# Kernel tuning notes

Hardware: AMD Instinct MI355X
Metric: run time of the kernel (lower is better)

Reference implementation:

```python
import jax, jax.numpy as jnp
import numpy as np

N = 50000
E = 600000
D_IN, D_HID, D_OUT = 128, 128, 64


def gcn_conv(x, edge_index, W, b):
    """PyG GCNConv: add self-loops, symmetric deg^{-1/2} normalization,
    linear transform, scatter-add aggregation, bias."""
    n = x.shape[0]
    loop = jnp.arange(n, dtype=edge_index.dtype)
    src = jnp.concatenate([edge_index[0], loop])
    dst = jnp.concatenate([edge_index[1], loop])
    h = x @ W  # [N, out]
    deg = jax.ops.segment_sum(jnp.ones_like(dst, dtype=h.dtype), dst, num_segments=n)
    dinv = jnp.where(deg > 0, jax.lax.rsqrt(jnp.maximum(deg, 1e-12)), 0.0)
    norm = dinv[src] * dinv[dst]  # [E+N]
    msg = h[src] * norm[:, None]  # gather + scale
    out = jax.ops.segment_sum(msg, dst, num_segments=n)  # scatter-add
    return out + b


def setup_inputs() -> dict:
    key = jax.random.key(0)
    k1, k2, k3, k4 = jax.random.split(key, 4)
    x = jax.random.normal(k1, (N, D_IN), dtype=jnp.float32)
    edge_index = jax.random.randint(k2, (2, E), 0, N, dtype=jnp.int64)
    s1 = (1.0 / np.sqrt(D_IN)).astype(np.float32) if False else np.float32(1.0 / np.sqrt(D_IN))
    s2 = np.float32(1.0 / np.sqrt(D_HID))
    W1 = jax.random.normal(k3, (D_IN, D_HID), dtype=jnp.float32) * s1
    b1 = jnp.zeros((D_HID,), dtype=jnp.float32)
    W2 = jax.random.normal(k4, (D_HID, D_OUT), dtype=jnp.float32) * s2
    b2 = jnp.zeros((D_OUT,), dtype=jnp.float32)
    return {"x": x, "edge_index": edge_index, "W1": W1, "b1": b1, "W2": W2, "b2": b2}


def reference(x, edge_index, W1, b1, W2, b2):
    # eval mode: dropout p = 0
    h = jax.nn.relu(gcn_conv(x, edge_index, W1, b1))
    return gcn_conv(h, edge_index, W2, b2)
```

## Files before the change

kernel.cpp:

```cpp
#include <hip/hip_runtime.h>
#include <hip/hip_fp16.h>
#include <stdint.h>

#define DIN 128
#define DHID 128
#define DOUT2 64

typedef __attribute__((ext_vector_type(8))) short short8v;
typedef __attribute__((ext_vector_type(4))) float f32x4;

__device__ __forceinline__ unsigned short f2bf(float f) {
    unsigned u = __float_as_uint(f);
    u += 0x7fffu + ((u >> 16) & 1u);
    return (unsigned short)(u >> 16);
}
__device__ __forceinline__ float bf2f(unsigned short b) {
    return __uint_as_float(((unsigned)b) << 16);
}
__device__ __forceinline__ float bflo(unsigned v) { return __uint_as_float(v << 16); }
__device__ __forceinline__ float bfhi(unsigned v) { return __uint_as_float(v & 0xffff0000u); }
__device__ __forceinline__ unsigned short f2h(float f) {
    return __half_as_ushort(__float2half_rn(f));
}
__device__ __forceinline__ float h2f(unsigned bits) {
    return __half2float(__ushort_as_half((unsigned short)bits));
}

__device__ __forceinline__ int detect_mode(const unsigned* ei) {
    int lane = threadIdx.x & 63;
    unsigned hi = ei[2 * lane + 1];
    return (__ballot(hi == 0u) == ~0ull) ? 1 : 0;
}

__global__ void prep_kernel(const float* __restrict__ W1, const float* __restrict__ W2,
                            unsigned short* __restrict__ wt1, unsigned short* __restrict__ wt2,
                            const int* ei32, const long long* ei64, unsigned* deg, int E) {
    if (blockIdx.x == 0) {
        for (int idx = threadIdx.x; idx < 128 * 128; idx += 256) {
            int n = idx & 127, k = idx >> 7;
            wt1[n * 128 + k] = f2bf(W1[idx]);
        }
    } else if (blockIdx.x == 1) {
        for (int idx = threadIdx.x; idx < 128 * 64; idx += 256) {
            int n = idx & 63, k = idx >> 6;
            wt2[n * 128 + k] = f2bf(W2[idx]);
        }
    } else {
        int mode = detect_mode((const unsigned*)ei32);
        int e = (blockIdx.x - 2) * 256 + threadIdx.x;
        if (e < E) {
            int d = mode ? (int)ei64[(size_t)E + e] : ei32[(size_t)E + e];
            atomicAdd(&deg[d], 1u);
        }
    }
}

template <int DO, typename AT>
__global__ __launch_bounds__(256) void gemm_mfma_kernel(const AT* __restrict__ A,
                                                        const unsigned short* __restrict__ Wt,
                                                        unsigned short* __restrict__ out,
                                                        int M) {
    constexpr int NT = DO / 16;
    __shared__ unsigned short As[64 * 136];
    const int tid = threadIdx.x;
    const int row0 = blockIdx.x * 64;

    if constexpr (sizeof(AT) == 4) {
        for (int idx = tid; idx < 64 * 32; idx += 256) {
            int r = idx >> 5, c4 = idx & 31;
            int row = row0 + r;
            ushort4 o = {0, 0, 0, 0};
            if (row < M) {
                float4 v = ((const float4*)A)[(size_t)row * 32 + c4];
                o.x = f2bf(v.x);
                o.y = f2bf(v.y);
                o.z = f2bf(v.z);
                o.w = f2bf(v.w);
            }
            *(ushort4*)&As[r * 136 + c4 * 4] = o;
        }
    } else {
        for (int idx = tid; idx < 64 * 16; idx += 256) {
            int r = idx >> 4, c8 = idx & 15;
            int row = row0 + r;
            uint4 v = {0u, 0u, 0u, 0u};
            if (row < M) v = ((const uint4*)A)[(size_t)row * 16 + c8];
            *(uint4*)&As[r * 136 + c8 * 8] = v;
        }
    }
    __syncthreads();

    const int wid = tid >> 6, lane = tid & 63;
    const int r16 = lane & 15, g = lane >> 4;
    f32x4 acc[NT];
#pragma unroll
    for (int n = 0; n < NT; n++) acc[n] = (f32x4){0.f, 0.f, 0.f, 0.f};

    const unsigned short* a_base = &As[(wid * 16 + r16) * 136 + g * 8];
    const unsigned short* b_base = Wt + r16 * 128 + g * 8;
#pragma unroll
    for (int kk = 0; kk < 4; kk++) {
        short8v a = *(const short8v*)(a_base + kk * 32);
#pragma unroll
        for (int n = 0; n < NT; n++) {
            short8v b = *(const short8v*)(b_base + n * 16 * 128 + kk * 32);
            acc[n] = __builtin_amdgcn_mfma_f32_16x16x32_bf16(a, b, acc[n], 0, 0, 0);
        }
    }

    const int rbase = row0 + wid * 16 + g * 4;
#pragma unroll
    for (int n = 0; n < NT; n++) {
#pragma unroll
        for (int q = 0; q < 4; q++) {
            int row = rbase + q;
            if (row < M) out[(size_t)row * DO + n * 16 + r16] = f2bf(acc[n][q]);
        }
    }
}

__global__ __launch_bounds__(256) void scan_blocksum_kernel(const unsigned* deg, int* bsum,
                                                            float* dinv, int N) {
    __shared__ int s[256];
    int t = threadIdx.x;
    int base = blockIdx.x * 1024 + t * 4;
    int sum = 0;
    if (base + 3 < N) {
        int4 v = *(const int4*)((const int*)deg + base);
        sum = v.x + v.y + v.z + v.w;
        float4 dv;
        dv.x = rsqrtf((float)(v.x + 1));
        dv.y = rsqrtf((float)(v.y + 1));
        dv.z = rsqrtf((float)(v.z + 1));
        dv.w = rsqrtf((float)(v.w + 1));
        *(float4*)(dinv + base) = dv;
    } else {
        for (int j = 0; j < 4; j++)
            if (base + j < N) {
                int d = (int)deg[base + j];
                sum += d;
                dinv[base + j] = rsqrtf((float)(d + 1));
            }
    }
    s[t] = sum;
    __syncthreads();
    for (int off = 128; off > 0; off >>= 1) {
        if (t < off) s[t] += s[t + off];
        __syncthreads();
    }
    if (t == 0) bsum[blockIdx.x] = s[0];
}

__global__ __launch_bounds__(256) void scan_bsum_kernel(int* bsum, int* row_ptr, int nb, int N) {
    __shared__ int s[256];
    int t = threadIdx.x;
    int v = (t < nb) ? bsum[t] : 0;
    s[t] = v;
    __syncthreads();
    for (int off = 1; off < 256; off <<= 1) {
        int u = (t >= off) ? s[t - off] : 0;
        __syncthreads();
        s[t] += u;
        __syncthreads();
    }
    if (t < nb) bsum[t] = s[t] - v;
    if (t == 255) row_ptr[N] = s[255];
}

__global__ __launch_bounds__(256) void scan_write_kernel(const unsigned* deg, const int* bsum,
                                                         int* row_ptr, int* cursor, int N) {
    __shared__ int s[256];
    int t = threadIdx.x;
    int base = blockIdx.x * 1024 + t * 4;
    int d[4];
    int sum = 0;
#pragma unroll
    for (int j = 0; j < 4; j++) {
        int idx = base + j;
        d[j] = (idx < N) ? (int)deg[idx] : 0;
        sum += d[j];
    }
    s[t] = sum;
    __syncthreads();
    for (int off = 1; off < 256; off <<= 1) {
        int u = (t >= off) ? s[t - off] : 0;
        __syncthreads();
        s[t] += u;
        __syncthreads();
    }
    int run = bsum[blockIdx.x] + s[t] - sum;
#pragma unroll
    for (int j = 0; j < 4; j++) {
        int idx = base + j;
        if (idx < N) {
            row_ptr[idx] = run;
            cursor[idx] = run;
            run += d[j];
        }
    }
}

__global__ void scatter_pack32_kernel(const int* ei32, const long long* ei64, const float* dinv,
                                      int* cursor, unsigned* csr, int E) {
    int mode = detect_mode((const unsigned*)ei32);
    int e = blockIdx.x * blockDim.x + threadIdx.x;
    if (e >= E) return;
    int s, d;
    if (mode) {
        s = (int)ei64[e];
        d = (int)ei64[(size_t)E + e];
    } else {
        s = ei32[e];
        d = ei32[(size_t)E + e];
    }
    int pos = atomicAdd(&cursor[d], 1);
    csr[pos] = (unsigned)s | ((unsigned)f2h(dinv[s]) << 16);
}

__global__ void scatter_pack64_kernel(const int* ei32, const long long* ei64, const float* dinv,
                                      int* cursor, unsigned long long* csr, int E) {
    int mode = detect_mode((const unsigned*)ei32);
    int e = blockIdx.x * blockDim.x + threadIdx.x;
    if (e >= E) return;
    int s, d;
    if (mode) {
        s = (int)ei64[e];
        d = (int)ei64[(size_t)E + e];
    } else {
        s = ei32[e];
        d = ei32[(size_t)E + e];
    }
    int pos = atomicAdd(&cursor[d], 1);
    csr[pos] = (unsigned long long)(unsigned)s |
               ((unsigned long long)__float_as_uint(dinv[s]) << 32);
}

__device__ __forceinline__ void unpack(unsigned p, int& s, float& w) {
    s = (int)(p & 0xffffu);
    w = h2f(p >> 16);
}
__device__ __forceinline__ void unpack(unsigned long long p, int& s, float& w) {
    s = (int)(unsigned)(p & 0xffffffffu);
    w = __uint_as_float((unsigned)(p >> 32));
}

template <int D, bool RELU, typename OT, typename CT>
__global__ __launch_bounds__(256) void agg_kernel(const unsigned short* __restrict__ h,
                                                  const CT* __restrict__ csr,
                                                  const int* __restrict__ row_ptr,
                                                  const float* __restrict__ dinv,
                                                  const float* __restrict__ bias,
                                                  OT* __restrict__ out, int N) {
    const int wid = threadIdx.x >> 6;
    const int lane = threadIdx.x & 63;
    const int i = blockIdx.x * 4 + wid;
    if (i >= N) return;
    const float di = dinv[i];
    const int start = row_ptr[i], end = row_ptr[i + 1];

    if constexpr (D == 128) {
        const unsigned* hu = (const unsigned*)h;
        unsigned sv = hu[(size_t)i * 64 + lane];
        float a0 = di * bflo(sv), b0 = di * bfhi(sv);
        float a1 = 0.f, b1 = 0.f, a2 = 0.f, b2 = 0.f, a3 = 0.f, b3 = 0.f;
        int j = start;
        for (; j + 8 <= end; j += 8) {
            int s[8];
            float w[8];
            unsigned v[8];
#pragma unroll
            for (int u = 0; u < 8; u++) unpack(csr[j + u], s[u], w[u]);
#pragma unroll
            for (int u = 0; u < 8; u++) v[u] = hu[(size_t)s[u] * 64 + lane];
            a0 = fmaf(w[0], bflo(v[0]), a0);
            b0 = fmaf(w[0], bfhi(v[0]), b0);
            a1 = fmaf(w[1], bflo(v[1]), a1);
            b1 = fmaf(w[1], bfhi(v[1]), b1);
            a2 = fmaf(w[2], bflo(v[2]), a2);
            b2 = fmaf(w[2], bfhi(v[2]), b2);
            a3 = fmaf(w[3], bflo(v[3]), a3);
            b3 = fmaf(w[3], bfhi(v[3]), b3);
            a0 = fmaf(w[4], bflo(v[4]), a0);
            b0 = fmaf(w[4], bfhi(v[4]), b0);
            a1 = fmaf(w[5], bflo(v[5]), a1);
            b1 = fmaf(w[5], bfhi(v[5]), b1);
            a2 = fmaf(w[6], bflo(v[6]), a2);
            b2 = fmaf(w[6], bfhi(v[6]), b2);
            a3 = fmaf(w[7], bflo(v[7]), a3);
            b3 = fmaf(w[7], bfhi(v[7]), b3);
        }
        for (; j < end; ++j) {
            int s0;
            float w0;
            unpack(csr[j], s0, w0);
            unsigned v0 = hu[(size_t)s0 * 64 + lane];
            a0 = fmaf(w0, bflo(v0), a0);
            b0 = fmaf(w0, bfhi(v0), b0);
        }
        float2 bv = ((const float2*)bias)[lane];
        float rx = di * ((a0 + a1) + (a2 + a3)) + bv.x;
        float ry = di * ((b0 + b1) + (b2 + b3)) + bv.y;
        if (RELU) {
            rx = fmaxf(rx, 0.f);
            ry = fmaxf(ry, 0.f);
        }
        if constexpr (sizeof(OT) == 2) {
            unsigned pv = (unsigned)f2bf(rx) | ((unsigned)f2bf(ry) << 16);
            ((unsigned*)out)[(size_t)i * 64 + lane] = pv;
        } else {
            ((float2*)out)[(size_t)i * 64 + lane] = make_float2(rx, ry);
        }
    } else {
        float a0 = di * bf2f(h[(size_t)i * 64 + lane]);
        float a1 = 0.f, a2 = 0.f, a3 = 0.f;
        int j = start;
        for (; j + 8 <= end; j += 8) {
            int s[8];
            float w[8];
            float v[8];
#pragma unroll
            for (int u = 0; u < 8; u++) unpack(csr[j + u], s[u], w[u]);
#pragma unroll
            for (int u = 0; u < 8; u++) v[u] = bf2f(h[(size_t)s[u] * 64 + lane]);
            a0 = fmaf(w[0], v[0], a0);
            a1 = fmaf(w[1], v[1], a1);
            a2 = fmaf(w[2], v[2], a2);
            a3 = fmaf(w[3], v[3], a3);
            a0 = fmaf(w[4], v[4], a0);
            a1 = fmaf(w[5], v[5], a1);
            a2 = fmaf(w[6], v[6], a2);
            a3 = fmaf(w[7], v[7], a3);
        }
        for (; j < end; ++j) {
            int s0;
            float w0;
            unpack(csr[j], s0, w0);
            a0 = fmaf(w0, bf2f(h[(size_t)s0 * 64 + lane]), a0);
        }
        float r = di * ((a0 + a1) + (a2 + a3)) + bias[lane];
        if (RELU) r = fmaxf(r, 0.f);
        if constexpr (sizeof(OT) == 2) {
            out[(size_t)i * 64 + lane] = (OT)f2bf(r);
        } else {
            out[(size_t)i * 64 + lane] = r;
        }
    }
}

extern "C" void kernel_launch(void* const* d_in, const int* in_sizes, int n_in,
                              void* d_out, int out_size, void* d_ws, size_t ws_size,
                              hipStream_t stream) {
    const float* x  = (const float*)d_in[0];
    const void*  ei = d_in[1];
    const float* W1 = (const float*)d_in[2];
    const float* b1 = (const float*)d_in[3];
    const float* W2 = (const float*)d_in[4];
    const float* b2 = (const float*)d_in[5];
    float* out = (float*)d_out;

    const int N = in_sizes[0] / DIN;
    const int E = in_sizes[1] / 2;

    char* ws = (char*)d_ws;
    size_t off = 0;
    auto alloc = [&](size_t bytes) -> void* {
        void* p = ws + off;
        off += (bytes + 255) & ~(size_t)255;
        return p;
    };
    unsigned*       deg  = (unsigned*)alloc((size_t)N * 4);
    float*          dinv = (float*)alloc((size_t)N * 4);
    int*            rowp = (int*)alloc((size_t)(N + 1) * 4);
    int*            curs = (int*)alloc((size_t)N * 4);
    int*            bsum = (int*)alloc(1024 * 4);
    unsigned short* wt1  = (unsigned short*)alloc(128 * 128 * 2);
    unsigned short* wt2  = (unsigned short*)alloc(128 * 64 * 2);
    void*           csr  = alloc((size_t)E * 8);
    unsigned short* h1   = (unsigned short*)alloc((size_t)N * DHID * 2);
    unsigned short* o1   = (unsigned short*)alloc((size_t)N * DHID * 2);
    unsigned short* h2   = h1;

    const int nb = (N + 1023) / 1024;
    const int gemmBlocks = (N + 63) / 64;
    const int degBlocks = (E + 255) / 256;

    hipMemsetAsync(deg, 0, (size_t)N * 4, stream);
    prep_kernel<<<2 + degBlocks, 256, 0, stream>>>(W1, W2, wt1, wt2, (const int*)ei,
                                                   (const long long*)ei, deg, E);
    gemm_mfma_kernel<DHID, float><<<gemmBlocks, 256, 0, stream>>>(x, wt1, h1, N);
    scan_blocksum_kernel<<<nb, 256, 0, stream>>>(deg, bsum, dinv, N);
    scan_bsum_kernel<<<1, 256, 0, stream>>>(bsum, rowp, nb, N);
    scan_write_kernel<<<nb, 256, 0, stream>>>(deg, bsum, rowp, curs, N);

    if (N <= 65535) {
        unsigned* csr32 = (unsigned*)csr;
        scatter_pack32_kernel<<<degBlocks, 256, 0, stream>>>((const int*)ei,
                                                             (const long long*)ei, dinv, curs,
                                                             csr32, E);
        agg_kernel<DHID, true, unsigned short, unsigned><<<(N + 3) / 4, 256, 0, stream>>>(
            h1, csr32, rowp, dinv, b1, o1, N);
        gemm_mfma_kernel<DOUT2, unsigned short><<<gemmBlocks, 256, 0, stream>>>(o1, wt2, h2, N);
        agg_kernel<DOUT2, false, float, unsigned><<<(N + 3) / 4, 256, 0, stream>>>(
            h2, csr32, rowp, dinv, b2, out, N);
    } else {
        unsigned long long* csr64 = (unsigned long long*)csr;
        scatter_pack64_kernel<<<degBlocks, 256, 0, stream>>>((const int*)ei,
                                                             (const long long*)ei, dinv, curs,
                                                             csr64, E);
        agg_kernel<DHID, true, unsigned short, unsigned long long><<<(N + 3) / 4, 256, 0,
                                                                     stream>>>(h1, csr64, rowp,
                                                                               dinv, b1, o1, N);
        gemm_mfma_kernel<DOUT2, unsigned short><<<gemmBlocks, 256, 0, stream>>>(o1, wt2, h2, N);
        agg_kernel<DOUT2, false, float, unsigned long long><<<(N + 3) / 4, 256, 0, stream>>>(
            h2, csr64, rowp, dinv, b2, out, N);
    }
}
```

Baseline: 247.4 us.

## Privatize degree and cursor counters into 8 block-group slots per node

Degree counting and CSR scatter now use NGRP=8 private counters per node, selected by block index, and the scan runs over the node-major 8x expanded array. Row pointers become the start of each node's first slot. The aim is to spread atomic contention on hot node counters across separate addresses. The cost is 8x larger deg, row-pointer and cursor arrays, a bigger memset, and the scan now handles one node per thread. The weight-transpose loops are also rewritten so the bf16 writes are contiguous.

After: 247.8 us. Within noise of the previous version (+0.1%).

```diff
diff --git a/kernel.cpp b/kernel.cpp
--- a/kernel.cpp
+++ b/kernel.cpp
@@ -5,6 +5,7 @@
 #define DIN 128
 #define DHID 128
 #define DOUT2 64
+#define NGRP 8
 
 typedef __attribute__((ext_vector_type(8))) short short8v;
 typedef __attribute__((ext_vector_type(4))) float f32x4;
@@ -34,23 +35,25 @@
 
 __global__ void prep_kernel(const float* __restrict__ W1, const float* __restrict__ W2,
                             unsigned short* __restrict__ wt1, unsigned short* __restrict__ wt2,
-                            const int* ei32, const long long* ei64, unsigned* deg, int E) {
+                            const int* ei32, const long long* ei64, unsigned* deg8, int E) {
     if (blockIdx.x == 0) {
         for (int idx = threadIdx.x; idx < 128 * 128; idx += 256) {
-            int n = idx & 127, k = idx >> 7;
-            wt1[n * 128 + k] = f2bf(W1[idx]);
+            int n = idx >> 7, k = idx & 127;
+            wt1[idx] = f2bf(W1[k * 128 + n]);
         }
     } else if (blockIdx.x == 1) {
-        for (int idx = threadIdx.x; idx < 128 * 64; idx += 256) {
-            int n = idx & 63, k = idx >> 6;
-            wt2[n * 128 + k] = f2bf(W2[idx]);
+        for (int idx = threadIdx.x; idx < 64 * 128; idx += 256) {
+            int n = idx >> 7, k = idx & 127;
+            wt2[idx] = f2bf(W2[k * 64 + n]);
         }
     } else {
         int mode = detect_mode((const unsigned*)ei32);
-        int e = (blockIdx.x - 2) * 256 + threadIdx.x;
+        int bi = blockIdx.x - 2;
+        int g = bi & (NGRP - 1);
+        int e = bi * 256 + threadIdx.x;
         if (e < E) {
             int d = mode ? (int)ei64[(size_t)E + e] : ei32[(size_t)E + e];
-            atomicAdd(&deg[d], 1u);
+            atomicAdd(&deg8[(size_t)d * NGRP + g], 1u);
         }
     }
 }
@@ -119,28 +122,17 @@
     }
 }
 
-__global__ __launch_bounds__(256) void scan_blocksum_kernel(const unsigned* deg, int* bsum,
+__global__ __launch_bounds__(256) void scan_blocksum_kernel(const unsigned* deg8, int* bsum,
                                                             float* dinv, int N) {
     __shared__ int s[256];
     int t = threadIdx.x;
-    int base = blockIdx.x * 1024 + t * 4;
+    int node = blockIdx.x * 256 + t;
     int sum = 0;
-    if (base + 3 < N) {
-        int4 v = *(const int4*)((const int*)deg + base);
-        sum = v.x + v.y + v.z + v.w;
-        float4 dv;
-        dv.x = rsqrtf((float)(v.x + 1));
-        dv.y = rsqrtf((float)(v.y + 1));
-        dv.z = rsqrtf((float)(v.z + 1));
-        dv.w = rsqrtf((float)(v.w + 1));
-        *(float4*)(dinv + base) = dv;
-    } else {
-        for (int j = 0; j < 4; j++)
-            if (base + j < N) {
-                int d = (int)deg[base + j];
-                sum += d;
-                dinv[base + j] = rsqrtf((float)(d + 1));
-            }
+    if (node < N) {
+        const int4* p = (const int4*)(deg8 + (size_t)node * NGRP);
+        int4 a = p[0], b = p[1];
+        sum = a.x + a.y + a.z + a.w + b.x + b.y + b.z + b.w;
+        dinv[node] = rsqrtf((float)(sum + 1));
     }
     s[t] = sum;
     __syncthreads();
@@ -151,7 +143,7 @@
     if (t == 0) bsum[blockIdx.x] = s[0];
 }
 
-__global__ __launch_bounds__(256) void scan_bsum_kernel(int* bsum, int* row_ptr, int nb, int N) {
+__global__ __launch_bounds__(256) void scan_bsum_kernel(int* bsum, int* rowp8, int nb, int M8) {
     __shared__ int s[256];
     int t = threadIdx.x;
     int v = (t < nb) ? bsum[t] : 0;
@@ -164,21 +156,26 @@
         __syncthreads();
     }
     if (t < nb) bsum[t] = s[t] - v;
-    if (t == 255) row_ptr[N] = s[255];
-}
-
-__global__ __launch_bounds__(256) void scan_write_kernel(const unsigned* deg, const int* bsum,
-                                                         int* row_ptr, int* cursor, int N) {
+    if (t == 255) rowp8[M8] = s[255];
+}
+
+__global__ __launch_bounds__(256) void scan_write_kernel(const unsigned* deg8, const int* bsum,
+                                                         int* rowp8, int* curs8, int N) {
     __shared__ int s[256];
     int t = threadIdx.x;
-    int base = blockIdx.x * 1024 + t * 4;
-    int d[4];
+    int node = blockIdx.x * 256 + t;
+    int d8[8];
     int sum = 0;
-#pragma unroll
-    for (int j = 0; j < 4; j++) {
-        int idx = base + j;
-        d[j] = (idx < N) ? (int)deg[idx] : 0;
-        sum += d[j];
+    if (node < N) {
+        const int4* p = (const int4*)(deg8 + (size_t)node * NGRP);
+        int4 a = p[0], b = p[1];
+        d8[0] = a.x; d8[1] = a.y; d8[2] = a.z; d8[3] = a.w;
+        d8[4] = b.x; d8[5] = b.y; d8[6] = b.z; d8[7] = b.w;
+#pragma unroll
+        for (int j = 0; j < 8; j++) sum += d8[j];
+    } else {
+#pragma unroll
+        for (int j = 0; j < 8; j++) d8[j] = 0;
     }
     s[t] = sum;
     __syncthreads();
@@ -189,20 +186,21 @@
         __syncthreads();
     }
     int run = bsum[blockIdx.x] + s[t] - sum;
-#pragma unroll
-    for (int j = 0; j < 4; j++) {
-        int idx = base + j;
-        if (idx < N) {
-            row_ptr[idx] = run;
-            cursor[idx] = run;
-            run += d[j];
+    if (node < N) {
+        size_t base = (size_t)node * NGRP;
+#pragma unroll
+        for (int j = 0; j < 8; j++) {
+            rowp8[base + j] = run;
+            curs8[base + j] = run;
+            run += d8[j];
         }
     }
 }
 
 __global__ void scatter_pack32_kernel(const int* ei32, const long long* ei64, const float* dinv,
-                                      int* cursor, unsigned* csr, int E) {
+                                      int* curs8, unsigned* csr, int E) {
     int mode = detect_mode((const unsigned*)ei32);
+    int g = blockIdx.x & (NGRP - 1);
     int e = blockIdx.x * blockDim.x + threadIdx.x;
     if (e >= E) return;
     int s, d;
@@ -213,13 +211,14 @@
         s = ei32[e];
         d = ei32[(size_t)E + e];
     }
-    int pos = atomicAdd(&cursor[d], 1);
+    int pos = atomicAdd(&curs8[(size_t)d * NGRP + g], 1);
     csr[pos] = (unsigned)s | ((unsigned)f2h(dinv[s]) << 16);
 }
 
 __global__ void scatter_pack64_kernel(const int* ei32, const long long* ei64, const float* dinv,
-                                      int* cursor, unsigned long long* csr, int E) {
+                                      int* curs8, unsigned long long* csr, int E) {
     int mode = detect_mode((const unsigned*)ei32);
+    int g = blockIdx.x & (NGRP - 1);
     int e = blockIdx.x * blockDim.x + threadIdx.x;
     if (e >= E) return;
     int s, d;
@@ -230,7 +229,7 @@
         s = ei32[e];
         d = ei32[(size_t)E + e];
     }
-    int pos = atomicAdd(&cursor[d], 1);
+    int pos = atomicAdd(&curs8[(size_t)d * NGRP + g], 1);
     csr[pos] = (unsigned long long)(unsigned)s |
                ((unsigned long long)__float_as_uint(dinv[s]) << 32);
 }
@@ -247,7 +246,7 @@
 template <int D, bool RELU, typename OT, typename CT>
 __global__ __launch_bounds__(256) void agg_kernel(const unsigned short* __restrict__ h,
                                                   const CT* __restrict__ csr,
-                                                  const int* __restrict__ row_ptr,
+                                                  const int* __restrict__ rowp8,
                                                   const float* __restrict__ dinv,
                                                   const float* __restrict__ bias,
                                                   OT* __restrict__ out, int N) {
@@ -256,7 +255,7 @@
     const int i = blockIdx.x * 4 + wid;
     if (i >= N) return;
     const float di = dinv[i];
-    const int start = row_ptr[i], end = row_ptr[i + 1];
+    const int start = rowp8[(size_t)i * NGRP], end = rowp8[(size_t)i * NGRP + NGRP];
 
     if constexpr (D == 128) {
         const unsigned* hu = (const unsigned*)h;
@@ -360,6 +359,7 @@
 
     const int N = in_sizes[0] / DIN;
     const int E = in_sizes[1] / 2;
+    const int M8 = N * NGRP;
 
     char* ws = (char*)d_ws;
     size_t off = 0;
@@ -368,50 +368,50 @@
         off += (bytes + 255) & ~(size_t)255;
         return p;
     };
-    unsigned*       deg  = (unsigned*)alloc((size_t)N * 4);
-    float*          dinv = (float*)alloc((size_t)N * 4);
-    int*            rowp = (int*)alloc((size_t)(N + 1) * 4);
-    int*            curs = (int*)alloc((size_t)N * 4);
-    int*            bsum = (int*)alloc(1024 * 4);
-    unsigned short* wt1  = (unsigned short*)alloc(128 * 128 * 2);
-    unsigned short* wt2  = (unsigned short*)alloc(128 * 64 * 2);
-    void*           csr  = alloc((size_t)E * 8);
-    unsigned short* h1   = (unsigned short*)alloc((size_t)N * DHID * 2);
-    unsigned short* o1   = (unsigned short*)alloc((size_t)N * DHID * 2);
-    unsigned short* h2   = h1;
-
-    const int nb = (N + 1023) / 1024;
+    unsigned*       deg8  = (unsigned*)alloc((size_t)M8 * 4);
+    float*          dinv  = (float*)alloc((size_t)N * 4);
+    int*            rowp8 = (int*)alloc((size_t)(M8 + 1) * 4);
+    int*            curs8 = (int*)alloc((size_t)M8 * 4);
+    int*            bsum  = (int*)alloc(1024 * 4);
+    unsigned short* wt1   = (unsigned short*)alloc(128 * 128 * 2);
+    unsigned short* wt2   = (unsigned short*)alloc(128 * 64 * 2);
+    void*           csr   = alloc((size_t)E * 8);
+    unsigned short* h1    = (unsigned short*)alloc((size_t)N * DHID * 2);
+    unsigned short* o1    = (unsigned short*)alloc((size_t)N * DHID * 2);
+    unsigned short* h2    = h1;
+
+    const int nb = (N + 255) / 256;
     const int gemmBlocks = (N + 63) / 64;
     const int degBlocks = (E + 255) / 256;
 
-    hipMemsetAsync(deg, 0, (size_t)N * 4, stream);
+    hipMemsetAsync(deg8, 0, (size_t)M8 * 4, stream);
     prep_kernel<<<2 + degBlocks, 256, 0, stream>>>(W1, W2, wt1, wt2, (const int*)ei,
-                                                   (const long long*)ei, deg, E);
+                                                   (const long long*)ei, deg8, E);
     gemm_mfma_kernel<DHID, float><<<gemmBlocks, 256, 0, stream>>>(x, wt1, h1, N);
-    scan_blocksum_kernel<<<nb, 256, 0, stream>>>(deg, bsum, dinv, N);
-    scan_bsum_kernel<<<1, 256, 0, stream>>>(bsum, rowp, nb, N);
-    scan_write_kernel<<<nb, 256, 0, stream>>>(deg, bsum, rowp, curs, N);
+    scan_blocksum_kernel<<<nb, 256, 0, stream>>>(deg8, bsum, dinv, N);
+    scan_bsum_kernel<<<1, 256, 0, stream>>>(bsum, rowp8, nb, M8);
+    scan_write_kernel<<<nb, 256, 0, stream>>>(deg8, bsum, rowp8, curs8, N);
 
     if (N <= 65535) {
         unsigned* csr32 = (unsigned*)csr;
         scatter_pack32_kernel<<<degBlocks, 256, 0, stream>>>((const int*)ei,
-                                                             (const long long*)ei, dinv, curs,
+                                                             (const long long*)ei, dinv, curs8,
                                                              csr32, E);
         agg_kernel<DHID, true, unsigned short, unsigned><<<(N + 3) / 4, 256, 0, stream>>>(
-            h1, csr32, rowp, dinv, b1, o1, N);
+            h1, csr32, rowp8, dinv, b1, o1, N);
         gemm_mfma_kernel<DOUT2, unsigned short><<<gemmBlocks, 256, 0, stream>>>(o1, wt2, h2, N);
         agg_kernel<DOUT2, false, float, unsigned><<<(N + 3) / 4, 256, 0, stream>>>(
-            h2, csr32, rowp, dinv, b2, out, N);
+            h2, csr32, rowp8, dinv, b2, out, N);
     } else {
         unsigned long long* csr64 = (unsigned long long*)csr;
         scatter_pack64_kernel<<<degBlocks, 256, 0, stream>>>((const int*)ei,
-                                                             (const long long*)ei, dinv, curs,
+                                                             (const long long*)ei, dinv, curs8,
                                                              csr64, E);
         agg_kernel<DHID, true, unsigned short, unsigned long long><<<(N + 3) / 4, 256, 0,
-                                                                     stream>>>(h1, csr64, rowp,
+                                                                     stream>>>(h1, csr64, rowp8,
                                                                                dinv, b1, o1, N);
         gemm_mfma_kernel<DOUT2, unsigned short><<<gemmBlocks, 256, 0, stream>>>(o1, wt2, h2, N);
         agg_kernel<DOUT2, false, float, unsigned long long><<<(N + 3) / 4, 256, 0, stream>>>(
-            h2, csr64, rowp, dinv, b2, out, N);
-    }
-}
+            h2, csr64, rowp8, dinv, b2, out, N);
+    }
+}
```
